# Performance work log

Hardware: AMD Instinct MI355X
Metric: run time of the kernel (lower is better)

The kernel has to match this reference:

```python
import jax, jax.numpy as jnp
import numpy as np

SLOPE = 25.0   # fast_sigmoid surrogate slope
BETA = 0.9     # LIF decay
THR = 1.0      # snntorch default threshold
STEPS = 10


@jax.custom_vjp
def spike(x):
    # Heaviside forward, fast-sigmoid surrogate backward
    return (x > 0).astype(x.dtype)

def _spike_fwd(x):
    return spike(x), x

def _spike_bwd(x, g):
    return (g / (SLOPE * jnp.abs(x) + 1.0) ** 2,)

spike.defvjp(_spike_fwd, _spike_bwd)


def lif(inp, mem):
    # snntorch Leaky, reset_mechanism='subtract': reset based on previous mem, detached
    reset = jax.lax.stop_gradient((mem > THR).astype(mem.dtype))
    mem = BETA * mem + inp - reset * THR
    spk = spike(mem - THR)
    return spk, mem


def setup_inputs() -> dict:
    key = jax.random.key(0)
    ks = jax.random.split(key, 4)
    B, IN, H, O = 65536, 512, 1024, 1
    x = jax.random.normal(ks[0], (B, IN), dtype=jnp.float32)
    W1 = jax.random.normal(ks[1], (IN, H), dtype=jnp.float32) / np.sqrt(IN)
    b1 = jnp.zeros((H,), jnp.float32)
    W2 = jax.random.normal(ks[2], (H, H), dtype=jnp.float32) / np.sqrt(H)
    b2 = jnp.zeros((H,), jnp.float32)
    Wo = jax.random.normal(ks[3], (H, O), dtype=jnp.float32) / np.sqrt(H)
    bo = jnp.zeros((O,), jnp.float32)
    return {"x": x, "W1": W1, "b1": b1, "W2": W2, "b2": b2, "Wo": Wo, "bo": bo}


def reference(x, W1, b1, W2, b2, Wo, bo):
    # fc1(x) is identical every timestep (x is static input current)
    cur1 = x @ W1 + b1                      # [B, H]
    B = x.shape[0]
    H = W1.shape[1]
    O = Wo.shape[1]
    m1 = jnp.zeros((B, H), x.dtype)
    m2 = jnp.zeros((B, H), x.dtype)
    mo = jnp.zeros((B, O), x.dtype)

    def step(carry, _):
        m1, m2, mo = carry
        s1, m1 = lif(cur1, m1)
        s2, m2 = lif(s1 @ W2 + b2, m2)
        _, mo = lif(s2 @ Wo + bo, mo)
        return (m1, m2, mo), mo

    _, recs = jax.lax.scan(step, (m1, m2, mo), None, length=STEPS)  # [STEPS, B, O]
    return recs.mean(0)
```

## Files before the change

### kernel.cpp

```cpp
#include <hip/hip_runtime.h>
#include <cstdint>
#include <cstddef>


typedef _Float16 f16;
typedef _Float16 f16x8 __attribute__((ext_vector_type(8)));
typedef float f32x4 __attribute__((ext_vector_type(4)));
typedef int i32x4 __attribute__((ext_vector_type(4)));
typedef unsigned int u32;

#define MFMA16(A, B, C) __builtin_amdgcn_mfma_f32_16x16x32_f16(A, B, C, 0, 0, 0)

static constexpr int BSZ = 65536;
static constexpr int IN = 512;
static constexpr int H = 1024;

__device__ __forceinline__ void gl_lds16(const void* g, void* l) {
    __builtin_amdgcn_global_load_lds(
        (const __attribute__((address_space(1))) u32*)g,
        (__attribute__((address_space(3))) u32*)l, 16, 0, 0);
}

__global__ void prep_dekker(const float* __restrict__ src, f16* __restrict__ dst) {
    int idx = blockIdx.x * 256 + threadIdx.x;
    int k = idx >> 10;
    int j = idx & 1023;
    float w = src[(size_t)k * 1024 + j];
    f16 hi = (f16)w;
    float lo = (w - (float)hi) * 2048.0f;
    size_t o = (size_t)j * 1024 + k;
    dst[o] = hi;
    dst[o + (size_t)H * H] = (f16)lo;
}

__global__ __launch_bounds__(256, 2) void k1_chain(
    const float* __restrict__ x, const float* __restrict__ w1,
    const float* __restrict__ b1, unsigned short* __restrict__ s1b) {
    __shared__ float xs[32][132];
    __shared__ float ws[32][256];
    const int hblk = blockIdx.x;
    const int bblk = blockIdx.y;
    const int tid = threadIdx.x;
    const int ht = tid & 15, bt = tid >> 4;
    const int h0 = hblk * 256, b0 = bblk * 128;

    float acc[8][16] = {};

    float4 xv[4], wv[8];
#pragma unroll
    for (int i = 0; i < 4; ++i) {
        int idx = tid + 256 * i;
        int br = idx >> 3, ks = idx & 7;
        xv[i] = *(const float4*)&x[(size_t)(b0 + br) * IN + ks * 4];
    }
#pragma unroll
    for (int i = 0; i < 8; ++i) {
        int idx = tid + 256 * i;
        int kr = idx >> 6, c4 = idx & 63;
        wv[i] = *(const float4*)&w1[(size_t)kr * H + h0 + c4 * 4];
    }

    for (int kc = 0; kc < 512; kc += 32) {
        __syncthreads();
#pragma unroll
        for (int i = 0; i < 4; ++i) {
            int idx = tid + 256 * i;
            int br = idx >> 3, ks = idx & 7;
            xs[ks * 4 + 0][br] = xv[i].x;
            xs[ks * 4 + 1][br] = xv[i].y;
            xs[ks * 4 + 2][br] = xv[i].z;
            xs[ks * 4 + 3][br] = xv[i].w;
        }
#pragma unroll
        for (int i = 0; i < 8; ++i) {
            int idx = tid + 256 * i;
            int kr = idx >> 6, c4 = idx & 63;
            *(float4*)&ws[kr][c4 * 4] = wv[i];
        }
        __syncthreads();
        int kn = (kc + 32) & 511;
#pragma unroll
        for (int i = 0; i < 4; ++i) {
            int idx = tid + 256 * i;
            int br = idx >> 3, ks = idx & 7;
            xv[i] = *(const float4*)&x[(size_t)(b0 + br) * IN + kn + ks * 4];
        }
#pragma unroll
        for (int i = 0; i < 8; ++i) {
            int idx = tid + 256 * i;
            int kr = idx >> 6, c4 = idx & 63;
            wv[i] = *(const float4*)&w1[(size_t)(kn + kr) * H + h0 + c4 * 4];
        }
#pragma unroll 2
        for (int k = 0; k < 32; ++k) {
            float xr[8];
            *(float4*)&xr[0] = *(const float4*)&xs[k][bt * 8];
            *(float4*)&xr[4] = *(const float4*)&xs[k][bt * 8 + 4];
            float wr[16];
#pragma unroll
            for (int g = 0; g < 4; ++g)
                *(float4*)&wr[g * 4] = *(const float4*)&ws[k][ht * 4 + 64 * g];
#pragma unroll
            for (int i = 0; i < 8; ++i)
#pragma unroll
                for (int j = 0; j < 16; ++j)
                    acc[i][j] = fmaf(xr[i], wr[j], acc[i][j]);
        }
    }

    float b1v[16];
#pragma unroll
    for (int g = 0; g < 4; ++g)
#pragma unroll
        for (int m = 0; m < 4; ++m)
            b1v[g * 4 + m] = b1[h0 + g * 64 + ht * 4 + m];
#pragma unroll
    for (int i = 0; i < 8; ++i) {
        unsigned short outb[16];
#pragma unroll
        for (int j = 0; j < 16; ++j) {
            float c = __fadd_rn(acc[i][j], b1v[j]);
            float m = 0.0f;
            unsigned bits = 0u;
#pragma unroll
            for (int t = 0; t < 10; ++t) {
                float rst = (m > 1.0f) ? 1.0f : 0.0f;
                m = __fmul_rn(0.9f, m);
                m = __fadd_rn(m, c);
                m = __fsub_rn(m, rst);
                if (m > 1.0f) bits |= (1u << t);
            }
            outb[j] = (unsigned short)bits;
        }
        size_t row = (size_t)(b0 + bt * 8 + i);
#pragma unroll
        for (int g = 0; g < 4; ++g)
            *(int2*)&s1b[row * H + h0 + g * 64 + ht * 4] = ((const int2*)outb)[g];
    }
}

__global__ __launch_bounds__(512, 4) void k2_spikes_gemm(
    const unsigned short* __restrict__ s1bits, const f16* __restrict__ w2d,
    const float* __restrict__ b2, const float* __restrict__ wo,
    float* __restrict__ po) {
    __shared__ __align__(16) char ldsraw[32768];
    i32x4 (*AL)[2][4][64]    = (i32x4 (*)[2][4][64])ldsraw;
    i32x4 (*BL)[2][2][2][64] = (i32x4 (*)[2][2][2][64])(ldsraw + 16384);
    double (*pvx)[10][4][16] = (double (*)[10][4][16])ldsraw;

    const int jblk = blockIdx.x, bblk = blockIdx.y;
    const int tid = threadIdx.x;
    const int lane = tid & 63, wave = tid >> 6;
    const int strip = wave & 3, cfw = wave >> 2;
    const int l15 = lane & 15, loct = lane >> 4;

    const bool stB = (wave >= 4);
    const int bp = (wave >> 1) & 1, bcf = wave & 1;
    const unsigned short* gA =
        s1bits + (size_t)(bblk * 64 + strip * 16 + l15) * 1024 + loct * 8;
    const f16* gB = w2d + (size_t)bp * H * H
                  + (size_t)(jblk * 32 + bcf * 16 + l15) * 1024 + loct * 8;

    f32x4 acc[10][2] = {};

    typedef union { i32x4 i; unsigned long long u[2]; f16x8 h; } U;

#define STAGE(t_)                                                        \
    do {                                                                 \
        int bi_ = (t_) & 1;                                              \
        int kk_ = ((t_) * 64) & 1023;                                    \
        if (stB) {                                                       \
            gl_lds16(gB + kk_,      &BL[bi_][0][bp][bcf][0]);            \
            gl_lds16(gB + kk_ + 32, &BL[bi_][1][bp][bcf][0]);            \
        } else {                                                         \
            gl_lds16(gA + kk_,      &AL[bi_][0][strip][0]);              \
            gl_lds16(gA + kk_ + 32, &AL[bi_][1][strip][0]);              \
        }                                                                \
    } while (0)

    STAGE(0);
    asm volatile("s_waitcnt vmcnt(0)" ::: "memory");
    __builtin_amdgcn_s_barrier();

    for (int t = 0; t < 16; ++t) {
        const int bi = t & 1;
        STAGE(t + 1);
#pragma unroll
        for (int kch = 0; kch < 2; ++kch) {
            U m;
            m.i = AL[bi][kch][strip][lane];
            U b0; b0.i = BL[bi][kch][0][cfw][lane];
            U b1; b1.i = BL[bi][kch][1][cfw][lane];
            f16x8 bf0 = b0.h, bf1 = b1.h;
            __builtin_amdgcn_s_setprio(1);
#pragma unroll
            for (int tt = 0; tt < 10; ++tt) {
                const int sh = 10 - tt;
                U r;
                r.u[0] = (m.u[0] << sh) & 0x0400040004000400ULL;
                r.u[1] = (m.u[1] << sh) & 0x0400040004000400ULL;
                acc[tt][0] = MFMA16(r.h, bf0, acc[tt][0]);
                acc[tt][1] = MFMA16(r.h, bf1, acc[tt][1]);
            }
            __builtin_amdgcn_s_setprio(0);
        }
        asm volatile("s_waitcnt vmcnt(0)" ::: "memory");
        __builtin_amdgcn_s_barrier();
    }
#undef STAGE

    int col0 = jblk * 32 + cfw * 16 + l15;
    float b2v = b2[col0];
    double wov = (double)wo[col0];
    float m2[4] = {0.0f, 0.0f, 0.0f, 0.0f};

#pragma unroll
    for (int tt = 0; tt < 10; ++tt) {
#pragma unroll
        for (int r = 0; r < 4; ++r) {
            float iv = (float)((double)acc[tt][0][r] * 16384.0 + (double)acc[tt][1][r] * 8.0);
            iv = __fadd_rn(iv, b2v);
            float rst = (m2[r] > 1.0f) ? 1.0f : 0.0f;
            m2[r] = __fmul_rn(0.9f, m2[r]);
            m2[r] = __fadd_rn(m2[r], iv);
            m2[r] = __fsub_rn(m2[r], rst);
            double pv = (m2[r] > 1.0f) ? wov : 0.0;
            pv += __shfl_xor(pv, 1);
            pv += __shfl_xor(pv, 2);
            pv += __shfl_xor(pv, 4);
            pv += __shfl_xor(pv, 8);
            if (l15 == r)
                pvx[cfw][tt][strip][loct * 4 + r] = pv;
        }
    }
    __syncthreads();
    for (int idx = tid; idx < 640; idx += 512) {
        int tt = idx >> 6, row = idx & 63;
        double v = pvx[0][tt][row >> 4][row & 15] + pvx[1][tt][row >> 4][row & 15];
        po[(size_t)(tt * 32 + jblk) * BSZ + bblk * 64 + row] = (float)v;
    }
}

__global__ void k3_out(const float* __restrict__ po, const float* __restrict__ bo,
                       float* __restrict__ out) {
    int b = blockIdx.x * 256 + threadIdx.x;
    float mo = 0.0f, s = 0.0f;
    float bov = bo[0];
    for (int t = 0; t < 10; ++t) {
        float inp = 0.0f;
#pragma unroll
        for (int jb = 0; jb < 32; ++jb) inp += po[(size_t)(t * 32 + jb) * BSZ + b];
        inp = __fadd_rn(inp, bov);
        float rst = (mo > 1.0f) ? 1.0f : 0.0f;
        mo = __fmul_rn(0.9f, mo);
        mo = __fadd_rn(mo, inp);
        mo = __fsub_rn(mo, rst);
        s += mo;
    }
    out[b] = s / 10.0f;
}

extern "C" void kernel_launch(void* const* d_in, const int* in_sizes, int n_in,
                              void* d_out, int out_size, void* d_ws, size_t ws_size,
                              hipStream_t stream) {
    (void)in_sizes; (void)n_in; (void)out_size; (void)ws_size;
    const float* x  = (const float*)d_in[0];
    const float* W1 = (const float*)d_in[1];
    const float* b1 = (const float*)d_in[2];
    const float* W2 = (const float*)d_in[3];
    const float* b2 = (const float*)d_in[4];
    const float* Wo = (const float*)d_in[5];
    const float* bo = (const float*)d_in[6];
    float* out = (float*)d_out;

    char* ws = (char*)d_ws;
    f16* w2d = (f16*)ws;
    unsigned short* s1bits = (unsigned short*)(ws + ((size_t)16 << 20));
    float* po = (float*)(ws + ((size_t)160 << 20));

    prep_dekker<<<dim3((H * H) / 256), 256, 0, stream>>>(W2, w2d);
    k1_chain<<<dim3(4, BSZ / 128), 256, 0, stream>>>(x, W1, b1, s1bits);
    k2_spikes_gemm<<<dim3(H / 32, BSZ / 64), 512, 0, stream>>>(s1bits, w2d, b2, Wo, po);
    k3_out<<<dim3(BSZ / 256), 256, 0, stream>>>(po, bo, out);
}
```

Measured before the change: 3.540 ms.

## Emit layer-2 spike bitmasks from GEMM and do Wo dot product in output kernel

The GEMM epilogue no longer does double-precision shuffle reductions against Wo and the LDS staging pass. It writes 16-bit ballot spike masks per column group instead, assembled into 32-bit words per 32 columns. The output kernel now loads Wo into shared memory and accumulates the weighted spike sum per row and timestep from those masks. This drops epilogue shuffles and the barrier, and keeps the intermediate buffer the same size. The cost is more bit-unpacking ALU work in k3, and the summation order changes from double to float.

```diff
diff --git a/kernel.cpp b/kernel.cpp
--- a/kernel.cpp
+++ b/kernel.cpp
@@ -141,12 +141,10 @@
 
 __global__ __launch_bounds__(512, 4) void k2_spikes_gemm(
     const unsigned short* __restrict__ s1bits, const f16* __restrict__ w2d,
-    const float* __restrict__ b2, const float* __restrict__ wo,
-    float* __restrict__ po) {
+    const float* __restrict__ b2, u32* __restrict__ po32) {
     __shared__ __align__(16) char ldsraw[32768];
     i32x4 (*AL)[2][4][64]    = (i32x4 (*)[2][4][64])ldsraw;
     i32x4 (*BL)[2][2][2][64] = (i32x4 (*)[2][2][2][64])(ldsraw + 16384);
-    double (*pvx)[10][4][16] = (double (*)[10][4][16])ldsraw;
 
     const int jblk = blockIdx.x, bblk = blockIdx.y;
     const int tid = threadIdx.x;
@@ -189,9 +187,9 @@
         for (int kch = 0; kch < 2; ++kch) {
             U m;
             m.i = AL[bi][kch][strip][lane];
-            U b0; b0.i = BL[bi][kch][0][cfw][lane];
-            U b1; b1.i = BL[bi][kch][1][cfw][lane];
-            f16x8 bf0 = b0.h, bf1 = b1.h;
+            U b0v; b0v.i = BL[bi][kch][0][cfw][lane];
+            U b1v; b1v.i = BL[bi][kch][1][cfw][lane];
+            f16x8 bf0 = b0v.h, bf1 = b1v.h;
             __builtin_amdgcn_s_setprio(1);
 #pragma unroll
             for (int tt = 0; tt < 10; ++tt) {
@@ -211,8 +209,8 @@
 
     int col0 = jblk * 32 + cfw * 16 + l15;
     float b2v = b2[col0];
-    double wov = (double)wo[col0];
     float m2[4] = {0.0f, 0.0f, 0.0f, 0.0f};
+    unsigned short* pw = (unsigned short*)po32;
 
 #pragma unroll
     for (int tt = 0; tt < 10; ++tt) {
@@ -224,36 +222,48 @@
             m2[r] = __fmul_rn(0.9f, m2[r]);
             m2[r] = __fadd_rn(m2[r], iv);
             m2[r] = __fsub_rn(m2[r], rst);
-            double pv = (m2[r] > 1.0f) ? wov : 0.0;
-            pv += __shfl_xor(pv, 1);
-            pv += __shfl_xor(pv, 2);
-            pv += __shfl_xor(pv, 4);
-            pv += __shfl_xor(pv, 8);
-            if (l15 == r)
-                pvx[cfw][tt][strip][loct * 4 + r] = pv;
-        }
-    }
+            unsigned long long bal = __ballot(m2[r] > 1.0f);
+            if (l15 == r) {
+                int row = bblk * 64 + strip * 16 + loct * 4 + r;
+                pw[(((size_t)jblk * 10 + tt) * BSZ + row) * 2 + cfw] =
+                    (unsigned short)(bal >> (loct * 16));
+            }
+        }
+    }
+}
+
+__global__ __launch_bounds__(256) void k3_out(
+    const u32* __restrict__ po32, const float* __restrict__ wo,
+    const float* __restrict__ bo, float* __restrict__ out) {
+    __shared__ float wos[1024];
+    const int tid = threadIdx.x;
+    for (int i = tid; i < 1024; i += 256) wos[i] = wo[i];
     __syncthreads();
-    for (int idx = tid; idx < 640; idx += 512) {
-        int tt = idx >> 6, row = idx & 63;
-        double v = pvx[0][tt][row >> 4][row & 15] + pvx[1][tt][row >> 4][row & 15];
-        po[(size_t)(tt * 32 + jblk) * BSZ + bblk * 64 + row] = (float)v;
-    }
-}
-
-__global__ void k3_out(const float* __restrict__ po, const float* __restrict__ bo,
-                       float* __restrict__ out) {
-    int b = blockIdx.x * 256 + threadIdx.x;
+    const int b = blockIdx.x * 256 + tid;
+
+    float inp[10] = {};
+    for (int jb = 0; jb < 32; ++jb) {
+        float wr[32];
+#pragma unroll
+        for (int g = 0; g < 8; ++g)
+            *(float4*)&wr[g * 4] = *(const float4*)&wos[jb * 32 + g * 4];
+#pragma unroll
+        for (int t = 0; t < 10; ++t) {
+            u32 mk = po32[((size_t)jb * 10 + t) * BSZ + b];
+#pragma unroll
+            for (int bit = 0; bit < 32; ++bit)
+                inp[t] += ((mk >> bit) & 1u) ? wr[bit] : 0.0f;
+        }
+    }
+
+    float bov = bo[0];
     float mo = 0.0f, s = 0.0f;
-    float bov = bo[0];
+#pragma unroll
     for (int t = 0; t < 10; ++t) {
-        float inp = 0.0f;
-#pragma unroll
-        for (int jb = 0; jb < 32; ++jb) inp += po[(size_t)(t * 32 + jb) * BSZ + b];
-        inp = __fadd_rn(inp, bov);
+        float iv = __fadd_rn(inp[t], bov);
         float rst = (mo > 1.0f) ? 1.0f : 0.0f;
         mo = __fmul_rn(0.9f, mo);
-        mo = __fadd_rn(mo, inp);
+        mo = __fadd_rn(mo, iv);
         mo = __fsub_rn(mo, rst);
         s += mo;
     }
@@ -276,10 +286,10 @@
     char* ws = (char*)d_ws;
     f16* w2d = (f16*)ws;
     unsigned short* s1bits = (unsigned short*)(ws + ((size_t)16 << 20));
-    float* po = (float*)(ws + ((size_t)160 << 20));
+    u32* po32 = (u32*)(ws + ((size_t)160 << 20));
 
     prep_dekker<<<dim3((H * H) / 256), 256, 0, stream>>>(W2, w2d);
     k1_chain<<<dim3(4, BSZ / 128), 256, 0, stream>>>(x, W1, b1, s1bits);
-    k2_spikes_gemm<<<dim3(H / 32, BSZ / 64), 512, 0, stream>>>(s1bits, w2d, b2, Wo, po);
-    k3_out<<<dim3(BSZ / 256), 256, 0, stream>>>(po, bo, out);
-}
+    k2_spikes_gemm<<<dim3(H / 32, BSZ / 64), 512, 0, stream>>>(s1bits, w2d, b2, po32);
+    k3_out<<<dim3(BSZ / 256), 256, 0, stream>>>(po32, Wo, bo, out);
+}
```

New measurement: 3.403 ms. -3.9%, faster.
